# Optimization experiments

Measured on AMD Instinct MI355X. Metric: run time of the kernel, lower is better.

Reference implementation:

```python
import jax, jax.numpy as jnp
import numpy as np

S_LEN, B, H, V, L = 128, 128, 1024, 32000, 2
H2 = 512  # ceil(H/2)
WSZ = 10
MAXW = 2 * WSZ + 1


def setup_inputs() -> dict:
    key = jax.random.key(0)
    k = jax.random.split(key, 16)
    def n(ki, shape, s=0.02):
        return jax.random.normal(ki, shape, dtype=jnp.float32) * s
    return {
        "source_sentence_length": S_LEN,
        "encoder_output": jax.random.normal(k[0], (S_LEN, B, H), dtype=jnp.float32),
        "word": jax.random.randint(k[1], (1, B), 0, V),
        "h0": jax.random.normal(k[2], (L, B, H), dtype=jnp.float32),
        "c0": jax.random.normal(k[3], (L, B, H), dtype=jnp.float32),
        "embedding": n(k[4], (V, H)),
        "lstm_Wih": n(k[5], (L, 4 * H, H)),
        "lstm_Whh": n(k[6], (L, 4 * H, H)),
        "lstm_bih": jnp.zeros((L, 4 * H), jnp.float32),
        "lstm_bhh": jnp.zeros((L, 4 * H), jnp.float32),
        "attn_w1": n(k[7], (H2, H)),
        "attn_b1": jnp.zeros((H2,), jnp.float32),
        "attn_w2": n(k[8], (1, H2)),
        "attn_b2": jnp.zeros((1,), jnp.float32),
        "fc1_w": n(k[9], (H, 2 * H)),
        "fc1_b": jnp.zeros((H,), jnp.float32),
        "fc2_w": n(k[10], (V, H)),
        "fc2_b": jnp.zeros((V,), jnp.float32),
    }


def reference(source_sentence_length, encoder_output, word, h0, c0, embedding,
              lstm_Wih, lstm_Whh, lstm_bih, lstm_bhh,
              attn_w1, attn_b1, attn_w2, attn_b2,
              fc1_w, fc1_b, fc2_w, fc2_b):
    S = source_sentence_length
    std2 = (WSZ / 2.0) ** 2  # std_squared from the module

    # embedding lookup: word [1,B] -> [1,B,H]; single-step multi-layer LSTM
    x = embedding[word][0]  # [B,H]
    hs, cs = [], []
    for l in range(h0.shape[0]):
        gates = x @ lstm_Wih[l].T + lstm_bih[l] + h0[l] @ lstm_Whh[l].T + lstm_bhh[l]
        i, f, g, o = jnp.split(gates, 4, axis=-1)
        c = jax.nn.sigmoid(f) * c0[l] + jax.nn.sigmoid(i) * jnp.tanh(g)
        h = jax.nn.sigmoid(o) * jnp.tanh(c)
        hs.append(h); cs.append(c); x = h
    h_new = jnp.stack(hs)
    c_new = jnp.stack(cs)
    out = x[None]  # decoder output [1,B,H]

    # predicted window center p in [0,S]
    p = S * jax.nn.sigmoid(jnp.tanh(out @ attn_w1.T + attn_b1) @ attn_w2.T + attn_b2)
    pb = p[0, :, 0]  # [B]
    ws = jnp.round(jnp.clip(pb - WSZ, 0, None)).astype(jnp.int32)
    we = jnp.round(jnp.clip(pb + WSZ, None, S - 1)).astype(jnp.int32)

    # windowed gather: position j of window b is source index ws[b]+j
    idx = ws[:, None] + jnp.arange(MAXW, dtype=jnp.int32)  # [B,MAXW]
    valid = idx <= we[:, None]
    enc_b = encoder_output.transpose(1, 0, 2)  # [B,S,H]
    h_s = jnp.take_along_axis(enc_b, jnp.clip(idx, 0, S - 1)[:, :, None], axis=1)
    h_s = jnp.where(valid[:, :, None], h_s, 0.0)  # zero-padded as in the torch code

    # faithful (non-negative, non-squared) gaussian term: exp((pos - p)/(2*std^2))
    gauss = jnp.where(valid, jnp.exp((idx.astype(enc_b.dtype) - pb[:, None]) / (2.0 * std2)), 0.0)

    scores = jnp.einsum('bh,bwh->bw', out[0], h_s)  # zero-padded slots score 0, kept in softmax
    a = jax.nn.softmax(scores, axis=-1) * gauss  # [B,MAXW]
    ctx = jnp.einsum('bw,bwh->bh', a, h_s)[None]  # [1,B,H]

    cat = jnp.concatenate([ctx, out], axis=2)  # [1,B,2H]
    o2 = jnp.tanh(cat @ fc1_w.T + fc1_b)
    y = jax.nn.log_softmax(o2 @ fc2_w.T + fc2_b, axis=2)  # [1,B,V]
    return (y, o2, h_new, c_new, a)
```

## Files before the change

### kernel.cpp

```cpp
#include <hip/hip_runtime.h>
#include <math.h>

namespace {

constexpr int B    = 128;
constexpr int H    = 1024;
constexpr int V    = 32000;
constexpr int WSZ  = 10;
constexpr int MAXW = 2 * WSZ + 1;

typedef __attribute__((ext_vector_type(8))) short bf16x8;
typedef __attribute__((ext_vector_type(4))) short short4v;
typedef __attribute__((ext_vector_type(4))) float f32x4;

__device__ __forceinline__ float sigf(float x) { return 1.0f / (1.0f + expf(-x)); }

__device__ __forceinline__ unsigned short rnebf(float f) {
    unsigned u = __float_as_uint(f);
    u += 0x7fffu + ((u >> 16) & 1u);
    return (unsigned short)(u >> 16);
}

__device__ __forceinline__ float bf2f(short s) {
    return __uint_as_float(((unsigned)(unsigned short)s) << 16);
}

__device__ __forceinline__ bf16x8 cvt8(const f32x4 a, const f32x4 b) {
    bf16x8 r;
    r[0] = (short)rnebf(a.x); r[1] = (short)rnebf(a.y);
    r[2] = (short)rnebf(a.z); r[3] = (short)rnebf(a.w);
    r[4] = (short)rnebf(b.x); r[5] = (short)rnebf(b.y);
    r[6] = (short)rnebf(b.z); r[7] = (short)rnebf(b.w);
    return r;
}

__device__ __forceinline__ void gl_lds16(const float* g, float* l) {
    __builtin_amdgcn_global_load_lds(
        (const __attribute__((address_space(1))) unsigned int*)g,
        (__attribute__((address_space(3))) unsigned int*)l,
        16, 0, 0);
}

struct S3 { short h, m, l; };

__device__ __forceinline__ S3 split3(float x) {
    S3 r;
    const unsigned uh = __float_as_uint(x) & 0xFFFF0000u;
    const float fh = __uint_as_float(uh);
    const float r1 = x - fh;
    const unsigned um = __float_as_uint(r1) & 0xFFFF0000u;
    const float fm = __uint_as_float(um);
    const float r2 = r1 - fm;
    const unsigned ul = __float_as_uint(r2) & 0xFFFF0000u;
    r.h = (short)(uh >> 16);
    r.m = (short)(um >> 16);
    r.l = (short)(ul >> 16);
    return r;
}

__device__ __forceinline__ void split8(const f32x4 a, const f32x4 b,
                                       bf16x8& wh, bf16x8& wm, bf16x8& wl) {
    S3 s;
    s = split3(a.x); wh[0] = s.h; wm[0] = s.m; wl[0] = s.l;
    s = split3(a.y); wh[1] = s.h; wm[1] = s.m; wl[1] = s.l;
    s = split3(a.z); wh[2] = s.h; wm[2] = s.m; wl[2] = s.l;
    s = split3(a.w); wh[3] = s.h; wm[3] = s.m; wl[3] = s.l;
    s = split3(b.x); wh[4] = s.h; wm[4] = s.m; wl[4] = s.l;
    s = split3(b.y); wh[5] = s.h; wm[5] = s.m; wl[5] = s.l;
    s = split3(b.z); wh[6] = s.h; wm[6] = s.m; wl[6] = s.l;
    s = split3(b.w); wh[7] = s.h; wm[7] = s.m; wl[7] = s.l;
}

__global__ __launch_bounds__(256, 2) void lstm_gemm(
    const short* __restrict__ Ah0, const short* __restrict__ Am0, const short* __restrict__ Al0,
    const short* __restrict__ Ah1, const short* __restrict__ Am1, const short* __restrict__ Al1,
    const float* __restrict__ W0, const float* __restrict__ W1,
    float* __restrict__ outbase)
{
    __shared__ float wt[2][4160];

    const int t    = threadIdx.x;
    const int lane = t & 63;
    const int w    = t >> 6;
    const int m16  = lane & 15;
    const int g    = lane >> 4;
    const int n0   = blockIdx.x * 64;
    const int y    = blockIdx.y;
    const int src  = y >> 2;
    const int k0   = (y & 3) * 256;
    const short* Ah = src ? Ah1 : Ah0;
    const short* Am = src ? Am1 : Am0;
    const short* Al = src ? Al1 : Al0;
    const float* W  = src ? W1  : W0;
    float* out = outbase + (size_t)y * 128 * 4096;

    bf16x8 ah[2][8], am[2][8], al[2][8];
    #pragma unroll
    for (int q = 0; q < 2; ++q) {
        const size_t ao = (size_t)((w * 2 + q) * 16 + m16) * 1024 + k0 + g * 8;
        #pragma unroll
        for (int s = 0; s < 8; ++s) {
            ah[q][s] = *(const bf16x8*)(Ah + ao + s * 32);
            am[q][s] = *(const bf16x8*)(Am + ao + s * 32);
            al[q][s] = *(const bf16x8*)(Al + ao + s * 32);
        }
    }

#define LSTM_STAGE(BUF, C)                                                  \
    {                                                                       \
        _Pragma("unroll")                                                   \
        for (int i = 0; i < 5; ++i) {                                       \
            const int idx = i * 256 + t;                                    \
            const int rr  = idx / 65;                                       \
            const int pp  = idx - rr * 65;                                  \
            if (idx < 1040 && pp < 64) {                                    \
                const float* s_ = W + (size_t)(n0 + (C) * 16 + rr) * 1024   \
                                + k0 + pp * 4;                              \
                gl_lds16(s_, &wt[BUF][(size_t)(i * 256 + w * 64) * 4]);     \
            }                                                               \
        }                                                                   \
    }

    LSTM_STAGE(0, 0)
    int cur = 0;
    #pragma unroll
    for (int c = 0; c < 4; ++c) {
        __syncthreads();
        if (c < 3) {
            if (cur == 0) LSTM_STAGE(1, c + 1)
            else          LSTM_STAGE(0, c + 1)
        }
        f32x4 acc0 = {}, acc1 = {};
        const float* lrow = &wt[cur][m16 * 260 + g * 8];
        #pragma unroll
        for (int s = 0; s < 8; ++s) {
            const f32x4 wa = *(const f32x4*)(lrow + s * 32);
            const f32x4 wb = *(const f32x4*)(lrow + s * 32 + 4);
            bf16x8 wh, wm, wl;
            split8(wa, wb, wh, wm, wl);
            acc0 = __builtin_amdgcn_mfma_f32_16x16x32_bf16(ah[0][s], wh, acc0, 0, 0, 0);
            acc0 = __builtin_amdgcn_mfma_f32_16x16x32_bf16(ah[0][s], wm, acc0, 0, 0, 0);
            acc0 = __builtin_amdgcn_mfma_f32_16x16x32_bf16(am[0][s], wh, acc0, 0, 0, 0);
            acc0 = __builtin_amdgcn_mfma_f32_16x16x32_bf16(ah[0][s], wl, acc0, 0, 0, 0);
            acc0 = __builtin_amdgcn_mfma_f32_16x16x32_bf16(am[0][s], wm, acc0, 0, 0, 0);
            acc0 = __builtin_amdgcn_mfma_f32_16x16x32_bf16(al[0][s], wh, acc0, 0, 0, 0);
            acc1 = __builtin_amdgcn_mfma_f32_16x16x32_bf16(ah[1][s], wh, acc1, 0, 0, 0);
            acc1 = __builtin_amdgcn_mfma_f32_16x16x32_bf16(ah[1][s], wm, acc1, 0, 0, 0);
            acc1 = __builtin_amdgcn_mfma_f32_16x16x32_bf16(am[1][s], wh, acc1, 0, 0, 0);
            acc1 = __builtin_amdgcn_mfma_f32_16x16x32_bf16(ah[1][s], wl, acc1, 0, 0, 0);
            acc1 = __builtin_amdgcn_mfma_f32_16x16x32_bf16(am[1][s], wm, acc1, 0, 0, 0);
            acc1 = __builtin_amdgcn_mfma_f32_16x16x32_bf16(al[1][s], wh, acc1, 0, 0, 0);
        }
        const int col = n0 + c * 16 + m16;
        #pragma unroll
        for (int j = 0; j < 4; ++j) {
            out[(size_t)(w * 32 + g * 4 + j) * 4096 + col]      = acc0[j];
            out[(size_t)(w * 32 + 16 + g * 4 + j) * 4096 + col] = acc1[j];
        }
        cur ^= 1;
    }
#undef LSTM_STAGE
}

__global__ __launch_bounds__(256) void fc2_gemm(
    const short* __restrict__ A, const float* __restrict__ W,
    short* __restrict__ outbase)
{
    __shared__ float wt[2][16 * 516];

    const int t    = threadIdx.x;
    const int lane = t & 63;
    const int w    = t >> 6;
    const int m16  = lane & 15;
    const int g    = lane >> 4;
    const int n0   = blockIdx.x * 64;
    const int y    = blockIdx.y;
    const int k0   = y * 512;
    short* out = outbase + (size_t)y * B * V;

    bf16x8 a[2][16];
    #pragma unroll
    for (int q = 0; q < 2; ++q) {
        const short* ap = A + (size_t)((w * 2 + q) * 16 + m16) * 1024 + k0 + g * 8;
        #pragma unroll
        for (int s = 0; s < 16; ++s)
            a[q][s] = *(const bf16x8*)(ap + s * 32);
    }

#define FC2_STAGE(BUF, C)                                                   \
    {                                                                       \
        _Pragma("unroll")                                                   \
        for (int i = 0; i < 9; ++i) {                                       \
            const int idx = i * 256 + t;                                    \
            const int rr  = idx / 129;                                      \
            const int pp  = idx - rr * 129;                                 \
            if (idx < 2064 && pp < 128) {                                   \
                const float* src = W + (size_t)(n0 + (C) * 16 + rr) * 1024  \
                                 + k0 + pp * 4;                             \
                gl_lds16(src, &wt[BUF][(size_t)(i * 256 + w * 64) * 4]);    \
            }                                                               \
        }                                                                   \
    }

    FC2_STAGE(0, 0)
    int cur = 0;
    #pragma unroll
    for (int c = 0; c < 4; ++c) {
        __syncthreads();
        if (c < 3) {
            if (cur == 0) FC2_STAGE(1, c + 1)
            else          FC2_STAGE(0, c + 1)
        }
        f32x4 acc0 = {}, acc1 = {};
        const float* lrow = &wt[cur][m16 * 516 + g * 8];
        #pragma unroll
        for (int s = 0; s < 16; ++s) {
            const f32x4 wa = *(const f32x4*)(lrow + s * 32);
            const f32x4 wb = *(const f32x4*)(lrow + s * 32 + 4);
            const bf16x8 bfr = cvt8(wa, wb);
            acc0 = __builtin_amdgcn_mfma_f32_16x16x32_bf16(a[0][s], bfr, acc0, 0, 0, 0);
            acc1 = __builtin_amdgcn_mfma_f32_16x16x32_bf16(a[1][s], bfr, acc1, 0, 0, 0);
        }
        const int col = n0 + c * 16 + m16;
        #pragma unroll
        for (int j = 0; j < 4; ++j) {
            out[(size_t)(w * 32 + g * 4 + j) * V + col]      = (short)rnebf(acc0[j]);
            out[(size_t)(w * 32 + 16 + g * 4 + j) * V + col] = (short)rnebf(acc1[j]);
        }
        cur ^= 1;
    }
#undef FC2_STAGE
}

__global__ __launch_bounds__(256, 2) void gemm_x3(
    const short* __restrict__ Ah0, const short* __restrict__ Am0, const short* __restrict__ Al0,
    const short* __restrict__ Ah1, const short* __restrict__ Am1, const short* __restrict__ Al1,
    const float* __restrict__ W0, const float* __restrict__ W1,
    int N, int Ksz, int ks_log2, float* __restrict__ outbase)
{
    const int y = blockIdx.y;
    const int src = y >> ks_log2;
    const short* Ah = src ? Ah1 : Ah0;
    const short* Am = src ? Am1 : Am0;
    const short* Al = src ? Al1 : Al0;
    const float* W  = src ? W1  : W0;
    const int k0 = (y & ((1 << ks_log2) - 1)) * Ksz;
    float* out = outbase + (size_t)y * 128 * N;

    const int t    = threadIdx.x;
    const int lane = t & 63;
    const int wv   = t >> 6;
    const int n0   = blockIdx.x * 64 + wv * 16;
    const int m16  = lane & 15;
    const int ko8  = (lane >> 4) * 8;

    const float* wp = W + (size_t)(n0 + m16) * 1024 + k0 + ko8;
    const size_t a0 = (size_t)m16 * 1024 + k0 + ko8;

    f32x4 acc[8] = {};

    f32x4 cwa = *(const f32x4*)(wp);      f32x4 cwb = *(const f32x4*)(wp + 4);
    f32x4 nwa = *(const f32x4*)(wp + 32); f32x4 nwb = *(const f32x4*)(wp + 36);

    for (int kc = 0; kc + 64 < Ksz; kc += 32) {
        bf16x8 ah[8], am[8], al[8];
        #pragma unroll
        for (int m = 0; m < 8; ++m) {
            const size_t ao = a0 + (size_t)m * 16384 + kc;
            ah[m] = *(const bf16x8*)(Ah + ao);
            am[m] = *(const bf16x8*)(Am + ao);
            al[m] = *(const bf16x8*)(Al + ao);
        }
        __builtin_amdgcn_sched_barrier(0);
        const f32x4 fwa = *(const f32x4*)(wp + kc + 64);
        const f32x4 fwb = *(const f32x4*)(wp + kc + 68);
        bf16x8 wh, wm, wl;
        split8(cwa, cwb, wh, wm, wl);
        #pragma unroll
        for (int m = 0; m < 8; ++m) {
            acc[m] = __builtin_amdgcn_mfma_f32_16x16x32_bf16(ah[m], wh, acc[m], 0, 0, 0);
            acc[m] = __builtin_amdgcn_mfma_f32_16x16x32_bf16(ah[m], wm, acc[m], 0, 0, 0);
            acc[m] = __builtin_amdgcn_mfma_f32_16x16x32_bf16(am[m], wh, acc[m], 0, 0, 0);
            acc[m] = __builtin_amdgcn_mfma_f32_16x16x32_bf16(ah[m], wl, acc[m], 0, 0, 0);
            acc[m] = __builtin_amdgcn_mfma_f32_16x16x32_bf16(am[m], wm, acc[m], 0, 0, 0);
            acc[m] = __builtin_amdgcn_mfma_f32_16x16x32_bf16(al[m], wh, acc[m], 0, 0, 0);
        }
        cwa = nwa; cwb = nwb; nwa = fwa; nwb = fwb;
    }
    #pragma unroll
    for (int tail = 0; tail < 2; ++tail) {
        const int kc = Ksz - 64 + tail * 32;
        bf16x8 ah[8], am[8], al[8];
        #pragma unroll
        for (int m = 0; m < 8; ++m) {
            const size_t ao = a0 + (size_t)m * 16384 + kc;
            ah[m] = *(const bf16x8*)(Ah + ao);
            am[m] = *(const bf16x8*)(Am + ao);
            al[m] = *(const bf16x8*)(Al + ao);
        }
        const f32x4 wa = tail ? nwa : cwa;
        const f32x4 wb = tail ? nwb : cwb;
        bf16x8 wh, wm, wl;
        split8(wa, wb, wh, wm, wl);
        #pragma unroll
        for (int m = 0; m < 8; ++m) {
            acc[m] = __builtin_amdgcn_mfma_f32_16x16x32_bf16(ah[m], wh, acc[m], 0, 0, 0);
            acc[m] = __builtin_amdgcn_mfma_f32_16x16x32_bf16(ah[m], wm, acc[m], 0, 0, 0);
            acc[m] = __builtin_amdgcn_mfma_f32_16x16x32_bf16(am[m], wh, acc[m], 0, 0, 0);
            acc[m] = __builtin_amdgcn_mfma_f32_16x16x32_bf16(ah[m], wl, acc[m], 0, 0, 0);
            acc[m] = __builtin_amdgcn_mfma_f32_16x16x32_bf16(am[m], wm, acc[m], 0, 0, 0);
            acc[m] = __builtin_amdgcn_mfma_f32_16x16x32_bf16(al[m], wh, acc[m], 0, 0, 0);
        }
    }

    #pragma unroll
    for (int m = 0; m < 8; ++m) {
        const int rbase = m * 16 + (lane >> 4) * 4;
        #pragma unroll
        for (int r = 0; r < 4; ++r)
            out[(size_t)(rbase + r) * N + n0 + m16] = acc[m][r];
    }
}

__global__ __launch_bounds__(256, 2) void fc1_gemm(
    const short* __restrict__ A0, const short* __restrict__ A1,
    const float* __restrict__ W, float* __restrict__ outbase)
{
    __shared__ float wt[2][16 * 132];

    const int t    = threadIdx.x;
    const int lane = t & 63;
    const int w    = t >> 6;
    const int m16  = lane & 15;
    const int g    = lane >> 4;
    const int n0   = blockIdx.x * 64;
    const int y    = blockIdx.y;
    const int src  = y >> 3;
    const int k0   = (y & 7) * 128;
    const int wk0  = src * 1024 + k0;
    const short* A = src ? A1 : A0;
    float* out = outbase + (size_t)y * 128 * 1024;

    bf16x8 a[2][4];
    #pragma unroll
    for (int q = 0; q < 2; ++q) {
        const short* ap = A + (size_t)((w * 2 + q) * 16 + m16) * 1024 + k0 + g * 8;
        #pragma unroll
        for (int s = 0; s < 4; ++s)
            a[q][s] = *(const bf16x8*)(ap + s * 32);
    }

#define FC1_STAGE(BUF, C)                                                   \
    {                                                                       \
        _Pragma("unroll")                                                   \
        for (int i = 0; i < 3; ++i) {                                       \
            const int idx = i * 256 + t;                                    \
            const int rr  = idx / 33;                                       \
            const int pp  = idx - rr * 33;                                  \
            if (idx < 528 && pp < 32) {                                     \
                const float* s_ = W + (size_t)(n0 + (C) * 16 + rr) * 2048   \
                                + wk0 + pp * 4;                             \
                gl_lds16(s_, &wt[BUF][(size_t)(i * 256 + w * 64) * 4]);     \
            }                                                               \
        }                                                                   \
    }

    FC1_STAGE(0, 0)
    int cur = 0;
    #pragma unroll
    for (int c = 0; c < 4; ++c) {
        __syncthreads();
        if (c < 3) {
            if (cur == 0) FC1_STAGE(1, c + 1)
            else          FC1_STAGE(0, c + 1)
        }
        f32x4 acc0 = {}, acc1 = {};
        const float* lrow = &wt[cur][m16 * 132 + g * 8];
        #pragma unroll
        for (int s = 0; s < 4; ++s) {
            const f32x4 wa = *(const f32x4*)(lrow + s * 32);
            const f32x4 wb = *(const f32x4*)(lrow + s * 32 + 4);
            const bf16x8 bfr = cvt8(wa, wb);
            acc0 = __builtin_amdgcn_mfma_f32_16x16x32_bf16(a[0][s], bfr, acc0, 0, 0, 0);
            acc1 = __builtin_amdgcn_mfma_f32_16x16x32_bf16(a[1][s], bfr, acc1, 0, 0, 0);
        }
        const int col = n0 + c * 16 + m16;
        #pragma unroll
        for (int j = 0; j < 4; ++j) {
            out[(size_t)(w * 32 + g * 4 + j) * 1024 + col]      = acc0[j];
            out[(size_t)(w * 32 + 16 + g * 4 + j) * 1024 + col] = acc1[j];
        }
        cur ^= 1;
    }
#undef FC1_STAGE
}

__global__ void prep_k(const int* __restrict__ word, const float* __restrict__ emb,
                       const float* __restrict__ h0,
                       short* __restrict__ xh, short* __restrict__ xm, short* __restrict__ xl,
                       short* __restrict__ h0h, short* __restrict__ h0m, short* __restrict__ h0l)
{
    const int blk = blockIdx.x, t = threadIdx.x;
    const float* src; short *dh, *dm, *dl; size_t off;
    if (blk < 128) {
        src = emb + (size_t)word[blk] * H; off = (size_t)blk * H;
        dh = xh; dm = xm; dl = xl;
    } else {
        const int i = blk - 128;
        src = h0 + (size_t)i * H; off = (size_t)i * H;
        dh = h0h; dm = h0m; dl = h0l;
    }
    const float4 v = ((const float4*)src)[t];
    short4v sh, sm, sl;
    S3 s;
    s = split3(v.x); sh.x = s.h; sm.x = s.m; sl.x = s.l;
    s = split3(v.y); sh.y = s.h; sm.y = s.m; sl.y = s.l;
    s = split3(v.z); sh.z = s.h; sm.z = s.m; sl.z = s.l;
    s = split3(v.w); sh.w = s.h; sm.w = s.m; sl.w = s.l;
    *(short4v*)(dh + off + t * 4) = sh;
    *(short4v*)(dm + off + t * 4) = sm;
    *(short4v*)(dl + off + t * 4) = sl;
}

__global__ void lstm_cell_k(const float* __restrict__ part,
                            const float* __restrict__ bih, const float* __restrict__ bhh,
                            const float* __restrict__ c0,
                            float* __restrict__ h_out, float* __restrict__ c_out,
                            short* __restrict__ xh, short* __restrict__ xm,
                            short* __restrict__ xl)
{
    const int idx = blockIdx.x * 256 + threadIdx.x;
    const int b = idx >> 10, hh = idx & 1023;
    const size_t base = (size_t)b * 4096;
    float g[4];
    #pragma unroll
    for (int j = 0; j < 4; ++j) {
        const int o = hh + j * H;
        float s = bih[o] + bhh[o];
        #pragma unroll
        for (int i = 0; i < 8; ++i) s += part[base + o + (size_t)i * 524288];
        g[j] = s;
    }
    const float c = sigf(g[1]) * c0[idx] + sigf(g[0]) * tanhf(g[2]);
    const float h = sigf(g[3]) * tanhf(c);
    c_out[idx] = c;
    h_out[idx] = h;
    const S3 s = split3(h);
    xh[idx] = s.h; xm[idx] = s.m; xl[idx] = s.l;
}

__global__ void attn_ctx_k(const float* __restrict__ part, const float* __restrict__ b1,
                           const float* __restrict__ w2v, const float* __restrict__ b2,
                           const int* __restrict__ Sptr,
                           const float* __restrict__ x, const float* __restrict__ enc,
                           float* __restrict__ a_out, short* __restrict__ ctxb)
{
    __shared__ float red[256];
    __shared__ float so[H];
    __shared__ float swred[4][MAXW];
    __shared__ float ssc[MAXW];
    __shared__ float sa[MAXW];
    __shared__ float sp;
    __shared__ int sw0, sw1;
    const int b = blockIdx.x, t = threadIdx.x;
    const int lane = t & 63, wvv = t >> 6;

    {
        const float* pa = part + (size_t)b * 512;
        float v = 0.f;
        #pragma unroll
        for (int jj = 0; jj < 2; ++jj) {
            const int j = t + jj * 256;
            float sgm = b1[j];
            #pragma unroll
            for (int i = 0; i < 16; ++i) sgm += pa[j + (size_t)i * 65536];
            v += tanhf(sgm) * w2v[j];
        }
        red[t] = v;
        __syncthreads();
        for (int s = 128; s > 0; s >>= 1) {
            if (t < s) red[t] += red[t + s];
            __syncthreads();
        }
        if (t == 0) {
            const float S = (float)Sptr[0];
            const float sv = S * sigf(red[0] + b2[0]);
            sp  = sv;
            sw0 = (int)rintf(fmaxf(sv - (float)WSZ, 0.f));
            sw1 = (int)rintf(fminf(sv + (float)WSZ, S - 1.f));
        }
    }
    for (int h = t; h < H; h += 256) so[h] = x[(size_t)b * H + h];
    __syncthreads();
    const int w0 = sw0, w1e = sw1;
    const float pbv = sp;

    float ps[MAXW];
    #pragma unroll
    for (int w = 0; w < MAXW; ++w) ps[w] = 0.f;
    for (int h4 = t; h4 < H / 4; h4 += 256) {
        const float4 o = ((const float4*)so)[h4];
        #pragma unroll
        for (int w = 0; w < MAXW; ++w) {
            const int idx = w0 + w;
            if (idx <= w1e) {
                const float4 e = *(const float4*)(enc + ((size_t)idx * B + b) * H + h4 * 4);
                ps[w] += o.x * e.x + o.y * e.y + o.z * e.z + o.w * e.w;
            }
        }
    }
    #pragma unroll
    for (int w = 0; w < MAXW; ++w) {
        float v = ps[w];
        for (int off = 32; off > 0; off >>= 1) v += __shfl_down(v, off);
        if (lane == 0) swred[wvv][w] = v;
    }
    __syncthreads();
    if (t == 0) {
        float m = -1e30f;
        for (int w = 0; w < MAXW; ++w) {
            const float s = swred[0][w] + swred[1][w] + swred[2][w] + swred[3][w];
            ssc[w] = s;
            m = fmaxf(m, s);
        }
        float den = 0.f;
        for (int w = 0; w < MAXW; ++w) den += expf(ssc[w] - m);
        for (int w = 0; w < MAXW; ++w) {
            const int idx = w0 + w;
            const float gauss = (idx <= w1e) ? expf(((float)idx - pbv) / 50.0f) : 0.f;
            sa[w] = expf(ssc[w] - m) / den * gauss;
        }
    }
    __syncthreads();
    if (t < MAXW) a_out[b * MAXW + t] = sa[t];
    for (int h4 = t; h4 < H / 4; h4 += 256) {
        float4 acc = {0.f, 0.f, 0.f, 0.f};
        #pragma unroll
        for (int w = 0; w < MAXW; ++w) {
            const int idx = w0 + w;
            if (idx <= w1e) {
                const float4 e = *(const float4*)(enc + ((size_t)idx * B + b) * H + h4 * 4);
                acc.x += sa[w] * e.x; acc.y += sa[w] * e.y;
                acc.z += sa[w] * e.z; acc.w += sa[w] * e.w;
            }
        }
        short4v s;
        s.x = (short)rnebf(acc.x); s.y = (short)rnebf(acc.y);
        s.z = (short)rnebf(acc.z); s.w = (short)rnebf(acc.w);
        *(short4v*)(ctxb + (size_t)b * H + h4 * 4) = s;
    }
}

__global__ void fc1_fin_k(const float* __restrict__ part, const float* __restrict__ bias,
                          float* __restrict__ o2, short* __restrict__ o2b)
{
    const int idx = blockIdx.x * 256 + threadIdx.x;
    const int n = idx & 1023;
    float v = bias[n];
    #pragma unroll
    for (int i = 0; i < 16; ++i) v += part[idx + (size_t)i * 131072];
    v = tanhf(v);
    o2[idx] = v;
    o2b[idx] = (short)rnebf(v);
}

__global__ __launch_bounds__(1024) void lsm_k(
    const short* __restrict__ p0, const short* __restrict__ p1,
    const float* __restrict__ bias, float* __restrict__ y)
{
    __shared__ float sm[16], ss[16], slse;
    const int b = blockIdx.x, t = threadIdx.x;
    const short* r0 = p0 + (size_t)b * V;
    const short* r1 = p1 + (size_t)b * V;
    float* yrow = y + (size_t)b * V;

    f32x4 r[8];
    float m = -1e30f, s = 0.f;
    #pragma unroll
    for (int i = 0; i < 8; ++i) {
        const int v4 = t + i * 1024;
        if (v4 < V / 4) {
            const short4v a = ((const short4v*)r0)[v4];
            const short4v c = ((const short4v*)r1)[v4];
            const f32x4 bv = ((const f32x4*)bias)[v4];
            f32x4 q;
            q.x = bf2f(a.x) + bf2f(c.x) + bv.x;
            q.y = bf2f(a.y) + bf2f(c.y) + bv.y;
            q.z = bf2f(a.z) + bf2f(c.z) + bv.z;
            q.w = bf2f(a.w) + bf2f(c.w) + bv.w;
            r[i] = q;
            const float mm = fmaxf(fmaxf(q.x, q.y), fmaxf(q.z, q.w));
            if (mm > m) { s *= expf(m - mm); m = mm; }
            s += expf(q.x - m) + expf(q.y - m) + expf(q.z - m) + expf(q.w - m);
        }
    }
    for (int off = 32; off > 0; off >>= 1) {
        const float mo = __shfl_down(m, off), so = __shfl_down(s, off);
        const float mn = fmaxf(m, mo);
        s = s * expf(m - mn) + so * expf(mo - mn);
        m = mn;
    }
    const int wv = t >> 6, lane = t & 63;
    if (lane == 0) { sm[wv] = m; ss[wv] = s; }
    __syncthreads();
    if (t == 0) {
        float M = sm[0], S = ss[0];
        for (int i = 1; i < 16; ++i) {
            const float mn = fmaxf(M, sm[i]);
            S = S * expf(M - mn) + ss[i] * expf(sm[i] - mn);
            M = mn;
        }
        slse = M + logf(S);
    }
    __syncthreads();
    const float lse = slse;
    #pragma unroll
    for (int i = 0; i < 8; ++i) {
        const int v4 = t + i * 1024;
        if (v4 < V / 4) {
            f32x4 q = r[i];
            q.x -= lse; q.y -= lse; q.z -= lse; q.w -= lse;
            ((f32x4*)yrow)[v4] = q;
        }
    }
}

}

extern "C" void kernel_launch(void* const* d_in, const int* in_sizes, int n_in,
                              void* d_out, int out_size, void* d_ws, size_t ws_size,
                              hipStream_t stream)
{
    const int*   Sp   = (const int*)d_in[0];
    const float* enc  = (const float*)d_in[1];
    const int*   word = (const int*)d_in[2];
    const float* h0   = (const float*)d_in[3];
    const float* c0   = (const float*)d_in[4];
    const float* emb  = (const float*)d_in[5];
    const float* Wih  = (const float*)d_in[6];
    const float* Whh  = (const float*)d_in[7];
    const float* bih  = (const float*)d_in[8];
    const float* bhh  = (const float*)d_in[9];
    const float* aw1  = (const float*)d_in[10];
    const float* ab1  = (const float*)d_in[11];
    const float* aw2  = (const float*)d_in[12];
    const float* ab2  = (const float*)d_in[13];
    const float* f1w  = (const float*)d_in[14];
    const float* f1b  = (const float*)d_in[15];
    const float* f2w  = (const float*)d_in[16];
    const float* f2b  = (const float*)d_in[17];

    float* outp = (float*)d_out;
    float* y    = outp;
    float* o2   = y  + (size_t)B * V;
    float* hN   = o2 + (size_t)B * H;
    float* cN   = hN + 2 * (size_t)B * H;
    float* aO   = cN + 2 * (size_t)B * H;

    char* wsp = (char*)d_ws;
    short* xh   = (short*)wsp;  wsp += (size_t)B * H * 2;
    short* xm   = (short*)wsp;  wsp += (size_t)B * H * 2;
    short* xl   = (short*)wsp;  wsp += (size_t)B * H * 2;
    short* h0h  = (short*)wsp;  wsp += (size_t)2 * B * H * 2;
    short* h0m  = (short*)wsp;  wsp += (size_t)2 * B * H * 2;
    short* h0l  = (short*)wsp;  wsp += (size_t)2 * B * H * 2;
    short* ctxb = (short*)wsp;  wsp += (size_t)B * H * 2;
    short* o2b  = (short*)wsp;  wsp += (size_t)B * H * 2;
    float* part = (float*)wsp;  wsp += (size_t)16 * B * 4 * H * 4;
    short* pf2  = (short*)wsp;  wsp += (size_t)2 * B * V * 2;

    prep_k<<<dim3(384), dim3(256), 0, stream>>>(word, emb, h0, xh, xm, xl, h0h, h0m, h0l);

    for (int l = 0; l < 2; ++l) {
        lstm_gemm<<<dim3(64, 8), dim3(256), 0, stream>>>(
            xh, xm, xl,
            h0h + (size_t)l * B * H, h0m + (size_t)l * B * H, h0l + (size_t)l * B * H,
            Wih + (size_t)l * 4 * H * H, Whh + (size_t)l * 4 * H * H,
            part);
        lstm_cell_k<<<dim3(B * H / 256), dim3(256), 0, stream>>>(
            part, bih + (size_t)l * 4 * H, bhh + (size_t)l * 4 * H,
            c0 + (size_t)l * B * H,
            hN + (size_t)l * B * H, cN + (size_t)l * B * H, xh, xm, xl);
    }

    const float* hfin = hN + (size_t)B * H;

    gemm_x3<<<dim3(8, 16), dim3(256), 0, stream>>>(
        xh, xm, xl, xh, xm, xl, aw1, aw1, 512, 64, 4, part);
    attn_ctx_k<<<dim3(B), dim3(256), 0, stream>>>(
        part, ab1, aw2, ab2, Sp, hfin, enc, aO, ctxb);

    fc1_gemm<<<dim3(16, 16), dim3(256), 0, stream>>>(ctxb, xh, f1w, part);
    fc1_fin_k<<<dim3(B * H / 256), dim3(256), 0, stream>>>(part, f1b, o2, o2b);

    fc2_gemm<<<dim3(V / 64, 2), dim3(256), 0, stream>>>(o2b, f2w, pf2);

    lsm_k<<<dim3(B), dim3(1024), 0, stream>>>(pf2, pf2 + (size_t)B * V, f2b, y);
}
```

Before: 165.6 us.

## Halve fc2 LDS stage size and raise occupancy with finer k-split pipelining

The fc2 GEMM now stages half-width (256-k) weight tiles, so its shared buffer shrinks from about 66KB to 33KB. This allows a launch-bounds hint of 4 blocks per CU. The 4-column-group loop becomes 8 stages, with two k-halves accumulated per column group. The first weight prefetch is issued before the A-fragment register loads so the two overlap. The cost is twice as many barriers and a tighter register budget under the 4-block bound, with the a[2][16] array held for the whole kernel, which could spill.

Result: slower. 208.6 us (+26.0%).

```diff
diff --git a/kernel.cpp b/kernel.cpp
--- a/kernel.cpp
+++ b/kernel.cpp
@@ -162,11 +162,11 @@
 #undef LSTM_STAGE
 }
 
-__global__ __launch_bounds__(256) void fc2_gemm(
+__global__ __launch_bounds__(256, 4) void fc2_gemm(
     const short* __restrict__ A, const float* __restrict__ W,
     short* __restrict__ outbase)
 {
-    __shared__ float wt[2][16 * 516];
+    __shared__ float wt[2][4160];
 
     const int t    = threadIdx.x;
     const int lane = t & 63;
@@ -178,56 +178,63 @@
     const int k0   = y * 512;
     short* out = outbase + (size_t)y * B * V;
 
-    bf16x8 a[2][16];
-    #pragma unroll
-    for (int q = 0; q < 2; ++q) {
-        const short* ap = A + (size_t)((w * 2 + q) * 16 + m16) * 1024 + k0 + g * 8;
-        #pragma unroll
-        for (int s = 0; s < 16; ++s)
-            a[q][s] = *(const bf16x8*)(ap + s * 32);
-    }
-
 #define FC2_STAGE(BUF, C)                                                   \
     {                                                                       \
         _Pragma("unroll")                                                   \
-        for (int i = 0; i < 9; ++i) {                                       \
+        for (int i = 0; i < 5; ++i) {                                       \
             const int idx = i * 256 + t;                                    \
-            const int rr  = idx / 129;                                      \
-            const int pp  = idx - rr * 129;                                 \
-            if (idx < 2064 && pp < 128) {                                   \
-                const float* src = W + (size_t)(n0 + (C) * 16 + rr) * 1024  \
-                                 + k0 + pp * 4;                             \
-                gl_lds16(src, &wt[BUF][(size_t)(i * 256 + w * 64) * 4]);    \
+            const int rr  = idx / 65;                                       \
+            const int pp  = idx - rr * 65;                                  \
+            if (idx < 1040 && pp < 64) {                                    \
+                const float* s_ = W                                         \
+                    + (size_t)(n0 + ((C) >> 1) * 16 + rr) * 1024            \
+                    + k0 + ((C) & 1) * 256 + pp * 4;                        \
+                gl_lds16(s_, &wt[BUF][(size_t)(i * 256 + w * 64) * 4]);     \
             }                                                               \
         }                                                                   \
     }
 
     FC2_STAGE(0, 0)
+
+    bf16x8 a[2][16];
+    #pragma unroll
+    for (int q = 0; q < 2; ++q) {
+        const short* ap = A + (size_t)((w * 2 + q) * 16 + m16) * 1024 + k0 + g * 8;
+        #pragma unroll
+        for (int s = 0; s < 16; ++s)
+            a[q][s] = *(const bf16x8*)(ap + s * 32);
+    }
+
     int cur = 0;
     #pragma unroll
-    for (int c = 0; c < 4; ++c) {
-        __syncthreads();
-        if (c < 3) {
-            if (cur == 0) FC2_STAGE(1, c + 1)
-            else          FC2_STAGE(0, c + 1)
-        }
+    for (int rg = 0; rg < 4; ++rg) {
         f32x4 acc0 = {}, acc1 = {};
-        const float* lrow = &wt[cur][m16 * 516 + g * 8];
-        #pragma unroll
-        for (int s = 0; s < 16; ++s) {
-            const f32x4 wa = *(const f32x4*)(lrow + s * 32);
-            const f32x4 wb = *(const f32x4*)(lrow + s * 32 + 4);
-            const bf16x8 bfr = cvt8(wa, wb);
-            acc0 = __builtin_amdgcn_mfma_f32_16x16x32_bf16(a[0][s], bfr, acc0, 0, 0, 0);
-            acc1 = __builtin_amdgcn_mfma_f32_16x16x32_bf16(a[1][s], bfr, acc1, 0, 0, 0);
-        }
-        const int col = n0 + c * 16 + m16;
+        #pragma unroll
+        for (int kh = 0; kh < 2; ++kh) {
+            __syncthreads();
+            const int next = rg * 2 + kh + 1;
+            if (next < 8) {
+                if (cur == 0) FC2_STAGE(1, next)
+                else          FC2_STAGE(0, next)
+            }
+            const float* lrow = &wt[cur][m16 * 260 + g * 8];
+            #pragma unroll
+            for (int s = 0; s < 8; ++s) {
+                const f32x4 wa = *(const f32x4*)(lrow + s * 32);
+                const f32x4 wb = *(const f32x4*)(lrow + s * 32 + 4);
+                const bf16x8 bfr = cvt8(wa, wb);
+                const int ks = kh * 8 + s;
+                acc0 = __builtin_amdgcn_mfma_f32_16x16x32_bf16(a[0][ks], bfr, acc0, 0, 0, 0);
+                acc1 = __builtin_amdgcn_mfma_f32_16x16x32_bf16(a[1][ks], bfr, acc1, 0, 0, 0);
+            }
+            cur ^= 1;
+        }
+        const int col = n0 + rg * 16 + m16;
         #pragma unroll
         for (int j = 0; j < 4; ++j) {
             out[(size_t)(w * 32 + g * 4 + j) * V + col]      = (short)rnebf(acc0[j]);
             out[(size_t)(w * 32 + 16 + g * 4 + j) * V + col] = (short)rnebf(acc1[j]);
         }
-        cur ^= 1;
     }
 #undef FC2_STAGE
 }
```
